# Kernel optimization log

Measured on AMD Instinct MI355X. Metric: run time of the kernel, lower is better.

Reference implementation:

```python
import jax, jax.numpy as jnp
import numpy as np

D = 256        # embedding dim (params[0])
V = 50000      # candidate vocab (params[1])
VW = 200000    # word vocab
B = 1024       # number of entities (batched ragged loop)
C = 64         # candidates per side (padded fixed length)
TOP_K = 10     # params[2]


def setup_inputs() -> dict:
    key = jax.random.key(0)
    ks = jax.random.split(key, 10)
    return {
        "word_l_ids": jax.random.randint(ks[0], (B,), 0, VW),
        "word_r_ids": jax.random.randint(ks[1], (B,), 0, VW),
        "cand_l_ids": jax.random.randint(ks[2], (B, C), 0, V),
        "cand_r_ids": jax.random.randint(ks[3], (B, C), 0, V),
        "word_embeds": jax.random.normal(ks[4], (VW, D), dtype=jnp.float32) * 0.1,
        "candidate_embeds": jax.random.normal(ks[5], (V, D), dtype=jnp.float32) * 0.1,
        # truncated_normal(stddev=0.5) for W_a, stddev=1.0 for W_c
        "W_a": jax.random.truncated_normal(ks[6], -2.0, 2.0, (D, D), dtype=jnp.float32) * 0.5,
        "b_a": jnp.zeros((1, D), dtype=jnp.float32),
        "W_c": jax.random.truncated_normal(ks[7], -2.0, 2.0, (2 * D, D), dtype=jnp.float32),
        "b_c": jnp.zeros((1, D), dtype=jnp.float32),
    }


def reference(word_l_ids, word_r_ids, cand_l_ids, cand_r_ids,
              word_embeds, candidate_embeds, W_a, b_a, W_c, b_c):
    # per-entity embedding lookups
    wl = word_embeds[word_l_ids]            # [B, D]
    wr = word_embeds[word_r_ids]            # [B, D]
    cl = candidate_embeds[cand_l_ids]       # [B, C, D]
    cr = candidate_embeds[cand_r_ids]       # [B, C, D]

    def attend(word, cands):
        # embed_word_align = tanh(word @ W_a + b_a)
        align = jnp.tanh(word @ W_a + b_a)                       # [B, D]
        # softmax over candidate axis (axis=0 in original per-entity view)
        scores = jnp.einsum("bcd,bd->bc", cands, align)          # [B, C]
        att = jax.nn.softmax(scores, axis=-1)                    # [B, C]
        # weighted sum of candidate embeddings
        return jnp.einsum("bc,bcd->bd", att, cands)              # [B, D]

    # note: left aggregation attends over RIGHT candidates and vice versa
    aggre_l = attend(wl, cr)
    aggre_r = attend(wr, cl)

    words_whole = wl + wr
    cands_whole = aggre_r + aggre_l
    phrase = jnp.tanh(jnp.concatenate([words_whole, cands_whole], axis=-1) @ W_c + b_c)  # [B, D]

    logits = phrase @ candidate_embeds.T    # [B, V]
    y_pred = jax.nn.softmax(logits, axis=-1)
    _, top_candidates = jax.lax.top_k(y_pred, TOP_K)             # [B, TOP_K]
    return y_pred, top_candidates
```

## Files before the change

### kernel.cpp

```cpp
#include <hip/hip_runtime.h>
#include <math.h>

#define DD 256
#define BB 1024
#define CC 64
#define VV 50000
#define TOPK 10
#define BM 128
#define BN 128
#define BK 64
#define LDK 72
#define NCHUNK 391
#define NMBLK 8
#define NWG (NCHUNK * NMBLK)
#define MAXCAND 60

typedef __attribute__((ext_vector_type(8))) short bf16x8;
typedef __attribute__((ext_vector_type(4))) float f32x4;

__device__ inline unsigned short f2bf(float x) {
    unsigned u = __float_as_uint(x);
    unsigned r = (u + 0x7FFFu + ((u >> 16) & 1u)) >> 16;
    return (unsigned short)r;
}

__global__ __launch_bounds__(256) void k_prep(
    const float* __restrict__ CE, unsigned short* __restrict__ CEb)
{
    const int i = blockIdx.x * 256 + threadIdx.x;
    const size_t base = (size_t)i * 8;
    if (base >= (size_t)VV * DD) return;
    const float4 a = *(const float4*)(CE + base);
    const float4 b = *(const float4*)(CE + base + 4);
    uint4 o;
    o.x = (unsigned)f2bf(a.x) | ((unsigned)f2bf(a.y) << 16);
    o.y = (unsigned)f2bf(a.z) | ((unsigned)f2bf(a.w) << 16);
    o.z = (unsigned)f2bf(b.x) | ((unsigned)f2bf(b.y) << 16);
    o.w = (unsigned)f2bf(b.z) | ((unsigned)f2bf(b.w) << 16);
    *(uint4*)(CEb + base) = o;
}

__global__ __launch_bounds__(256) void k_phrase(
    const int* __restrict__ wl_ids, const int* __restrict__ wr_ids,
    const int* __restrict__ cl_ids, const int* __restrict__ cr_ids,
    const float* __restrict__ WE, const float* __restrict__ CE,
    const float* __restrict__ W_a, const float* __restrict__ b_a,
    const float* __restrict__ W_c, const float* __restrict__ b_c,
    float* __restrict__ phrase, unsigned short* __restrict__ phraseb)
{
    const int b = blockIdx.x;
    const int t = threadIdx.x;
    __shared__ float s_wl[DD], s_wr[DD], s_align[DD], s_agg0[DD], s_agg1[DD];
    __shared__ float s_part[256];
    __shared__ float s_att[CC];
    __shared__ int s_rid[CC];

    s_wl[t] = WE[(size_t)wl_ids[b] * DD + t];
    s_wr[t] = WE[(size_t)wr_ids[b] * DD + t];
    __syncthreads();

    for (int side = 0; side < 2; ++side) {
        const float* w    = (side == 0) ? s_wl : s_wr;
        const int*   cids = (side == 0) ? (cr_ids + b * CC) : (cl_ids + b * CC);

        float acc = b_a[t];
        #pragma unroll 4
        for (int k = 0; k < DD; ++k) acc = fmaf(w[k], W_a[k * DD + t], acc);
        s_align[t] = tanhf(acc);
        if (t < CC) s_rid[t] = cids[t];
        __syncthreads();

        {
            const int c = t & 63, p = t >> 6;
            const float* crow = CE + (size_t)s_rid[c] * DD + p * 64;
            const float* al = s_align + p * 64;
            float sc = 0.f;
            #pragma unroll 4
            for (int j = 0; j < 64; ++j) sc = fmaf(crow[j], al[j], sc);
            s_part[t] = sc;
        }
        __syncthreads();
        if (t < CC) {
            float s = s_part[t] + s_part[64 + t] + s_part[128 + t] + s_part[192 + t];
            float m = s;
            for (int off = 32; off; off >>= 1) m = fmaxf(m, __shfl_xor(m, off, 64));
            float e = expf(s - m);
            float sum = e;
            for (int off = 32; off; off >>= 1) sum += __shfl_xor(sum, off, 64);
            s_att[t] = e / sum;
        }
        __syncthreads();
        {
            float ag = 0.f;
            #pragma unroll 4
            for (int c = 0; c < CC; ++c)
                ag = fmaf(s_att[c], CE[(size_t)s_rid[c] * DD + t], ag);
            if (side == 0) s_agg0[t] = ag; else s_agg1[t] = ag;
        }
        __syncthreads();
    }

    s_wl[t]  += s_wr[t];
    s_agg0[t] += s_agg1[t];
    __syncthreads();

    float acc = b_c[t];
    #pragma unroll 4
    for (int k = 0; k < DD; ++k) acc = fmaf(s_wl[k],  W_c[k * DD + t], acc);
    #pragma unroll 4
    for (int k = 0; k < DD; ++k) acc = fmaf(s_agg0[k], W_c[(DD + k) * DD + t], acc);
    const float ph = tanhf(acc);
    phrase[b * DD + t] = ph;
    phraseb[b * DD + t] = f2bf(ph);
}

template<bool STATS, bool BF16CE>
__global__ __launch_bounds__(256) void k_gemm(
    const unsigned short* __restrict__ phraseb,
    const float* __restrict__ CE, const unsigned short* __restrict__ CEb,
    float* __restrict__ out,
    float* __restrict__ pmax, float* __restrict__ psum,
    const float* __restrict__ rowM, const float* __restrict__ rowInvS,
    const float* __restrict__ rowTh,
    int* __restrict__ cand_idx, int* __restrict__ cand_cnt)
{
    __shared__ unsigned short sA[BM * LDK];
    __shared__ unsigned short sB[BN * LDK];

    const int t = threadIdx.x;
    const int wave = t >> 6, lane = t & 63;
    const int wm = wave >> 1, wn = wave & 1;
    const int quad = lane >> 4, l15 = lane & 15;

    const int wg = blockIdx.x;
    const int q  = (wg & 7) * NCHUNK + (wg >> 3);
    const int m0 = (q & 7) * BM;
    const int cn = q >> 3;
    const int n0 = cn * BN;

    f32x4 acc[4][4] = {};

    for (int k0 = 0; k0 < DD; k0 += BK) {
        __syncthreads();
        #pragma unroll
        for (int r = 0; r < 4; ++r) {
            const int idx = t + r * 256;
            const int m = idx >> 3, k8 = (idx & 7) * 8;
            const uint4 v = *(const uint4*)(phraseb + (size_t)(m0 + m) * DD + k0 + k8);
            *(uint4*)(sA + m * LDK + k8) = v;
        }
        if constexpr (BF16CE) {
            #pragma unroll
            for (int r = 0; r < 4; ++r) {
                const int idx = t + r * 256;
                const int n = idx >> 3, k8 = (idx & 7) * 8;
                const int gn = n0 + n;
                uint4 v = make_uint4(0u, 0u, 0u, 0u);
                if (gn < VV) v = *(const uint4*)(CEb + (size_t)gn * DD + k0 + k8);
                *(uint4*)(sB + n * LDK + k8) = v;
            }
        } else {
            #pragma unroll
            for (int r = 0; r < 8; ++r) {
                const int idx = t + r * 256;
                const int n = idx >> 4, k4 = (idx & 15) * 4;
                const int gn = n0 + n;
                float4 v = make_float4(0.f, 0.f, 0.f, 0.f);
                if (gn < VV) v = *(const float4*)(CE + (size_t)gn * DD + k0 + k4);
                ushort4 h;
                h.x = f2bf(v.x); h.y = f2bf(v.y); h.z = f2bf(v.z); h.w = f2bf(v.w);
                *(ushort4*)(sB + n * LDK + k4) = h;
            }
        }
        __syncthreads();
        #pragma unroll
        for (int kk = 0; kk < BK; kk += 32) {
            bf16x8 af[4], bfr[4];
            #pragma unroll
            for (int i = 0; i < 4; ++i) {
                af[i]  = *(const bf16x8*)(sA + (wm * 64 + i * 16 + l15) * LDK + kk + quad * 8);
                bfr[i] = *(const bf16x8*)(sB + (wn * 64 + i * 16 + l15) * LDK + kk + quad * 8);
            }
            #pragma unroll
            for (int i = 0; i < 4; ++i)
                #pragma unroll
                for (int j = 0; j < 4; ++j)
                    acc[i][j] = __builtin_amdgcn_mfma_f32_16x16x32_bf16(af[i], bfr[j], acc[i][j], 0, 0, 0);
        }
    }

    bool val[4];
    #pragma unroll
    for (int j = 0; j < 4; ++j) val[j] = (n0 + wn * 64 + j * 16 + l15) < VV;

    if constexpr (STATS) {
        __shared__ float sM[2][BM], sS[2][BM];
        #pragma unroll
        for (int i = 0; i < 4; ++i) {
            #pragma unroll
            for (int r = 0; r < 4; ++r) {
                float m1 = -INFINITY;
                #pragma unroll
                for (int j = 0; j < 4; ++j) if (val[j]) m1 = fmaxf(m1, acc[i][j][r]);
                #pragma unroll
                for (int off = 8; off >= 1; off >>= 1) m1 = fmaxf(m1, __shfl_xor(m1, off, 64));
                float s = 0.f;
                #pragma unroll
                for (int j = 0; j < 4; ++j) if (val[j]) s += __expf(acc[i][j][r] - m1);
                #pragma unroll
                for (int off = 8; off >= 1; off >>= 1) s += __shfl_xor(s, off, 64);
                if (l15 == 0) {
                    const int mloc = wm * 64 + i * 16 + quad * 4 + r;
                    sM[wn][mloc] = m1;
                    sS[wn][mloc] = s;
                }
            }
        }
        __syncthreads();
        if (t < BM) {
            const float Ma = sM[0][t], Mb = sM[1][t];
            const float nM = fmaxf(Ma, Mb);
            const float S  = sS[0][t] * __expf(Ma - nM) + sS[1][t] * __expf(Mb - nM);
            const size_t o = (size_t)(m0 + t) * NCHUNK + cn;
            pmax[o] = nM;
            psum[o] = S;
        }
    } else {
        __shared__ float sMr[BM], sIr[BM], sTr[BM];
        if (t < BM) {
            sMr[t] = rowM[m0 + t];
            sIr[t] = rowInvS[m0 + t];
            sTr[t] = rowTh[m0 + t];
        }
        __syncthreads();
        #pragma unroll
        for (int i = 0; i < 4; ++i) {
            #pragma unroll
            for (int r = 0; r < 4; ++r) {
                const int ml = wm * 64 + i * 16 + quad * 4 + r;
                const int gm = m0 + ml;
                const float M = sMr[ml], inv = sIr[ml], th = sTr[ml];
                #pragma unroll
                for (int j = 0; j < 4; ++j) {
                    if (val[j]) {
                        const int gn = n0 + wn * 64 + j * 16 + l15;
                        const float y = __expf(acc[i][j][r] - M) * inv;
                        __builtin_nontemporal_store(y, out + (size_t)gm * VV + gn);
                        if (y >= th) {
                            const int p = atomicAdd(&cand_cnt[gm], 1);
                            if (p < MAXCAND) cand_idx[gm * MAXCAND + p] = gn;
                        }
                    }
                }
            }
        }
    }
}

__global__ __launch_bounds__(64) void k_rowstats(
    const float* __restrict__ pmax, const float* __restrict__ psum,
    float* __restrict__ rowM, float* __restrict__ rowInvS, float* __restrict__ rowTh,
    int* __restrict__ cand_cnt)
{
    const int b = blockIdx.x, t = threadIdx.x;
    float M = -INFINITY, S = 0.f;
    float top[TOPK];
    #pragma unroll
    for (int j = 0; j < TOPK; ++j) top[j] = -INFINITY;

    for (int c = t; c < NCHUNK; c += 64) {
        const float m = pmax[(size_t)b * NCHUNK + c];
        const float s = psum[(size_t)b * NCHUNK + c];
        const float nM = fmaxf(M, m);
        S = S * __expf(M - nM) + s * __expf(m - nM);
        M = nM;
        if (m > top[TOPK - 1]) {
            float v = m;
            #pragma unroll
            for (int p = 0; p < TOPK; ++p) {
                const float hi = fmaxf(top[p], v), lo = fminf(top[p], v);
                top[p] = hi; v = lo;
            }
        }
    }
    #pragma unroll
    for (int off = 32; off; off >>= 1) {
        const float m2 = __shfl_xor(M, off, 64);
        const float s2 = __shfl_xor(S, off, 64);
        const float nM = fmaxf(M, m2);
        S = S * __expf(M - nM) + s2 * __expf(m2 - nM);
        M = nM;
    }
    float v10 = -INFINITY;
    for (int k = 0; k < TOPK; ++k) {
        float g = top[0];
        #pragma unroll
        for (int off = 32; off; off >>= 1) g = fmaxf(g, __shfl_xor(g, off, 64));
        v10 = g;
        const unsigned long long mk = __ballot(top[0] == g);
        if (mk && t == __ffsll(mk) - 1) {
            #pragma unroll
            for (int p = 0; p < TOPK - 1; ++p) top[p] = top[p + 1];
            top[TOPK - 1] = -INFINITY;
        }
    }
    if (t == 0) {
        rowM[b] = M;
        const float inv = 1.f / S;
        rowInvS[b] = inv;
        rowTh[b] = 0.90f * __expf(v10 - M) * inv;
        cand_cnt[b] = 0;
    }
}

__global__ __launch_bounds__(64) void k_rescore(
    const float* __restrict__ phrase, const float* __restrict__ CE,
    const int* __restrict__ cand_idx, const int* __restrict__ cand_cnt,
    float* __restrict__ topk_out)
{
    const int b = blockIdx.x, lane = threadIdx.x;
    int cnt = cand_cnt[b];
    if (cnt > MAXCAND) cnt = MAXCAND;
    __shared__ float s_val[MAXCAND];
    __shared__ int   s_idx[MAXCAND];

    if (lane < MAXCAND) { s_val[lane] = -INFINITY; s_idx[lane] = 0x7ffffff0; }
    __syncthreads();

    const float4 ph = *(const float4*)(phrase + (size_t)b * DD + lane * 4);
    for (int c = 0; c < cnt; ++c) {
        const int id = cand_idx[b * MAXCAND + c];
        const float4 ce = *(const float4*)(CE + (size_t)id * DD + lane * 4);
        float d = ph.x * ce.x + ph.y * ce.y + ph.z * ce.z + ph.w * ce.w;
        #pragma unroll
        for (int off = 32; off; off >>= 1) d += __shfl_xor(d, off, 64);
        if (lane == 0) { s_val[c] = d; s_idx[c] = id; }
    }
    __syncthreads();
    if (lane == 0) {
        for (int j = 0; j < TOPK; ++j) {
            int best = j;
            for (int c = j + 1; c < cnt; ++c) {
                if (s_val[c] > s_val[best] ||
                    (s_val[c] == s_val[best] && s_idx[c] < s_idx[best])) best = c;
            }
            const float bv = s_val[best]; const int bi = s_idx[best];
            s_val[best] = s_val[j]; s_idx[best] = s_idx[j];
            s_val[j] = bv; s_idx[j] = bi;
            topk_out[b * TOPK + j] = (float)bi;
        }
    }
}

extern "C" void kernel_launch(void* const* d_in, const int* in_sizes, int n_in,
                              void* d_out, int out_size, void* d_ws, size_t ws_size,
                              hipStream_t stream) {
    const int*   wl_ids = (const int*)d_in[0];
    const int*   wr_ids = (const int*)d_in[1];
    const int*   cl_ids = (const int*)d_in[2];
    const int*   cr_ids = (const int*)d_in[3];
    const float* WE     = (const float*)d_in[4];
    const float* CE     = (const float*)d_in[5];
    const float* W_a    = (const float*)d_in[6];
    const float* b_a    = (const float*)d_in[7];
    const float* W_c    = (const float*)d_in[8];
    const float* b_c    = (const float*)d_in[9];

    float* out = (float*)d_out;
    float* ws  = (float*)d_ws;

    float* phrase  = ws;
    unsigned short* phraseb = (unsigned short*)(ws + 262144);
    float* pmax    = ws + 262144 + 131072;
    float* psum    = pmax + (size_t)BB * NCHUNK;
    float* rowM    = psum + (size_t)BB * NCHUNK;
    float* rowInvS = rowM + BB;
    float* rowTh   = rowInvS + BB;
    int*   cand_idx = (int*)(rowTh + BB);
    int*   cand_cnt = cand_idx + (size_t)BB * MAXCAND;
    float* topk_out = out + (size_t)BB * VV;

    const size_t baseBytes = (size_t)((char*)(cand_cnt + BB) - (char*)ws);
    const size_t ceOff = (baseBytes + 255) & ~(size_t)255;
    const bool bf16ce = ws_size >= ceOff + (size_t)VV * DD * 2;
    unsigned short* CEb = (unsigned short*)((char*)ws + ceOff);

    k_phrase<<<BB, 256, 0, stream>>>(wl_ids, wr_ids, cl_ids, cr_ids,
                                     WE, CE, W_a, b_a, W_c, b_c, phrase, phraseb);
    if (bf16ce) {
        k_prep<<<(VV * DD / 8 + 255) / 256, 256, 0, stream>>>(CE, CEb);
        k_gemm<true, true><<<NWG, 256, 0, stream>>>(phraseb, CE, CEb, out,
            pmax, psum, rowM, rowInvS, rowTh, cand_idx, cand_cnt);
        k_rowstats<<<BB, 64, 0, stream>>>(pmax, psum, rowM, rowInvS, rowTh, cand_cnt);
        k_gemm<false, true><<<NWG, 256, 0, stream>>>(phraseb, CE, CEb, out,
            pmax, psum, rowM, rowInvS, rowTh, cand_idx, cand_cnt);
    } else {
        k_gemm<true, false><<<NWG, 256, 0, stream>>>(phraseb, CE, CEb, out,
            pmax, psum, rowM, rowInvS, rowTh, cand_idx, cand_cnt);
        k_rowstats<<<BB, 64, 0, stream>>>(pmax, psum, rowM, rowInvS, rowTh, cand_cnt);
        k_gemm<false, false><<<NWG, 256, 0, stream>>>(phraseb, CE, CEb, out,
            pmax, psum, rowM, rowInvS, rowTh, cand_idx, cand_cnt);
    }
    k_rescore<<<BB, 64, 0, stream>>>(phrase, CE, cand_idx, cand_cnt, topk_out);
}
```

Measured before the change: 696.0 us.

## Split phrase kernel into batched align, attention, and phrase GEMM kernels

```diff
diff --git a/kernel.cpp b/kernel.cpp
--- a/kernel.cpp
+++ b/kernel.cpp
@@ -112,6 +112,178 @@
     const float ph = tanhf(acc);
     phrase[b * DD + t] = ph;
     phraseb[b * DD + t] = f2bf(ph);
+}
+
+__global__ __launch_bounds__(256) void k_align(
+    const int* __restrict__ wl_ids, const int* __restrict__ wr_ids,
+    const float* __restrict__ WE,
+    const float* __restrict__ W_a, const float* __restrict__ b_a,
+    float* __restrict__ alignbuf, float* __restrict__ wordsum)
+{
+    __shared__ float sA[32][260];
+    __shared__ int s_id[32];
+
+    const int t  = threadIdx.x;
+    const int rt = blockIdx.x >> 2;
+    const int cg = blockIdx.x & 3;
+    const int b0 = rt * 16;
+    const int s0 = rt * 32;
+
+    if (t < 32) {
+        const int e = b0 + (t >> 1);
+        s_id[t] = (t & 1) ? wr_ids[e] : wl_ids[e];
+    }
+    __syncthreads();
+
+    #pragma unroll 8
+    for (int r = 0; r < 32; ++r)
+        sA[r][t] = WE[(size_t)s_id[r] * DD + t];
+    __syncthreads();
+
+    if (cg == 0) {
+        #pragma unroll
+        for (int i = 0; i < 16; ++i)
+            wordsum[(size_t)(b0 + i) * DD + t] = sA[2 * i][t] + sA[2 * i + 1][t];
+    }
+
+    const int c = t & 63, mg = t >> 6;
+    const int col = cg * 64 + c;
+    const float ba = b_a[col];
+    float acc[8];
+    #pragma unroll
+    for (int j = 0; j < 8; ++j) acc[j] = ba;
+
+    for (int k4 = 0; k4 < 64; ++k4) {
+        const int kb = k4 * 4;
+        const float w0 = W_a[(size_t)(kb + 0) * DD + col];
+        const float w1 = W_a[(size_t)(kb + 1) * DD + col];
+        const float w2 = W_a[(size_t)(kb + 2) * DD + col];
+        const float w3 = W_a[(size_t)(kb + 3) * DD + col];
+        #pragma unroll
+        for (int j = 0; j < 8; ++j) {
+            const float4 a = *(const float4*)&sA[mg * 8 + j][kb];
+            acc[j] = fmaf(a.x, w0, acc[j]);
+            acc[j] = fmaf(a.y, w1, acc[j]);
+            acc[j] = fmaf(a.z, w2, acc[j]);
+            acc[j] = fmaf(a.w, w3, acc[j]);
+        }
+    }
+    #pragma unroll
+    for (int j = 0; j < 8; ++j)
+        alignbuf[(size_t)(s0 + mg * 8 + j) * DD + col] = tanhf(acc[j]);
+}
+
+__global__ __launch_bounds__(256) void k_attn(
+    const int* __restrict__ cl_ids, const int* __restrict__ cr_ids,
+    const float* __restrict__ CE, const float* __restrict__ alignbuf,
+    float* __restrict__ aggsum)
+{
+    __shared__ float sC[CC][260];
+    __shared__ float sAl[DD];
+    __shared__ float s_part[256];
+    __shared__ float s_att[CC];
+    __shared__ int s_rid[CC];
+
+    const int b = blockIdx.x;
+    const int t = threadIdx.x;
+    float agg_acc = 0.f;
+
+    for (int side = 0; side < 2; ++side) {
+        const int* cids = (side == 0) ? (cr_ids + b * CC) : (cl_ids + b * CC);
+        if (t < CC) s_rid[t] = cids[t];
+        sAl[t] = alignbuf[(size_t)(2 * b + side) * DD + t];
+        __syncthreads();
+
+        #pragma unroll 8
+        for (int r = 0; r < CC; ++r)
+            sC[r][t] = CE[(size_t)s_rid[r] * DD + t];
+        __syncthreads();
+
+        {
+            const int c = t & 63, p = t >> 6;
+            float sc = 0.f;
+            #pragma unroll
+            for (int jj = 0; jj < 16; ++jj) {
+                const float4 v  = *(const float4*)&sC[c][p * 64 + 4 * jj];
+                const float4 al = *(const float4*)&sAl[p * 64 + 4 * jj];
+                sc = fmaf(v.x, al.x, sc);
+                sc = fmaf(v.y, al.y, sc);
+                sc = fmaf(v.z, al.z, sc);
+                sc = fmaf(v.w, al.w, sc);
+            }
+            s_part[t] = sc;
+        }
+        __syncthreads();
+        if (t < CC) {
+            float s = s_part[t] + s_part[64 + t] + s_part[128 + t] + s_part[192 + t];
+            float m = s;
+            for (int off = 32; off; off >>= 1) m = fmaxf(m, __shfl_xor(m, off, 64));
+            float e = expf(s - m);
+            float sum = e;
+            for (int off = 32; off; off >>= 1) sum += __shfl_xor(sum, off, 64);
+            s_att[t] = e / sum;
+        }
+        __syncthreads();
+        {
+            float ag = 0.f;
+            #pragma unroll 8
+            for (int c = 0; c < CC; ++c)
+                ag = fmaf(s_att[c], sC[c][t], ag);
+            agg_acc += ag;
+        }
+        __syncthreads();
+    }
+    aggsum[(size_t)b * DD + t] = agg_acc;
+}
+
+__global__ __launch_bounds__(256) void k_phrase2(
+    const float* __restrict__ wordsum, const float* __restrict__ aggsum,
+    const float* __restrict__ W_c, const float* __restrict__ b_c,
+    float* __restrict__ phrase, unsigned short* __restrict__ phraseb)
+{
+    __shared__ float sX[16][516];
+
+    const int t  = threadIdx.x;
+    const int rt = blockIdx.x >> 2;
+    const int cg = blockIdx.x & 3;
+    const int b0 = rt * 16;
+
+    #pragma unroll
+    for (int i = 0; i < 16; ++i) {
+        sX[i][t]       = wordsum[(size_t)(b0 + i) * DD + t];
+        sX[i][DD + t]  = aggsum [(size_t)(b0 + i) * DD + t];
+    }
+    __syncthreads();
+
+    const int c = t & 63, mg = t >> 6;
+    const int col = cg * 64 + c;
+    const float bc = b_c[col];
+    float acc[4];
+    #pragma unroll
+    for (int j = 0; j < 4; ++j) acc[j] = bc;
+
+    for (int k4 = 0; k4 < 128; ++k4) {
+        const int kb = k4 * 4;
+        const float w0 = W_c[(size_t)(kb + 0) * DD + col];
+        const float w1 = W_c[(size_t)(kb + 1) * DD + col];
+        const float w2 = W_c[(size_t)(kb + 2) * DD + col];
+        const float w3 = W_c[(size_t)(kb + 3) * DD + col];
+        #pragma unroll
+        for (int j = 0; j < 4; ++j) {
+            const float4 a = *(const float4*)&sX[mg * 4 + j][kb];
+            acc[j] = fmaf(a.x, w0, acc[j]);
+            acc[j] = fmaf(a.y, w1, acc[j]);
+            acc[j] = fmaf(a.z, w2, acc[j]);
+            acc[j] = fmaf(a.w, w3, acc[j]);
+        }
+    }
+    #pragma unroll
+    for (int j = 0; j < 4; ++j) {
+        const int b = b0 + mg * 4 + j;
+        const float ph = tanhf(acc[j]);
+        phrase[(size_t)b * DD + col] = ph;
+        phraseb[(size_t)b * DD + col] = f2bf(ph);
+    }
 }
 
 template<bool STATS, bool BF16CE>
@@ -381,12 +553,25 @@
     float* topk_out = out + (size_t)BB * VV;
 
     const size_t baseBytes = (size_t)((char*)(cand_cnt + BB) - (char*)ws);
-    const size_t ceOff = (baseBytes + 255) & ~(size_t)255;
+
+    float* alignbuf = (float*)((char*)ws + baseBytes);
+    float* wordsum  = alignbuf + (size_t)2 * BB * DD;
+    float* aggsum   = wordsum + (size_t)BB * DD;
+    const size_t ext1End = baseBytes + (size_t)4 * BB * DD * 4;
+    const bool newphrase = ws_size >= ext1End;
+
+    const size_t ceOff = ((newphrase ? ext1End : baseBytes) + 255) & ~(size_t)255;
     const bool bf16ce = ws_size >= ceOff + (size_t)VV * DD * 2;
     unsigned short* CEb = (unsigned short*)((char*)ws + ceOff);
 
-    k_phrase<<<BB, 256, 0, stream>>>(wl_ids, wr_ids, cl_ids, cr_ids,
-                                     WE, CE, W_a, b_a, W_c, b_c, phrase, phraseb);
+    if (newphrase) {
+        k_align<<<256, 256, 0, stream>>>(wl_ids, wr_ids, WE, W_a, b_a, alignbuf, wordsum);
+        k_attn<<<BB, 256, 0, stream>>>(cl_ids, cr_ids, CE, alignbuf, aggsum);
+        k_phrase2<<<256, 256, 0, stream>>>(wordsum, aggsum, W_c, b_c, phrase, phraseb);
+    } else {
+        k_phrase<<<BB, 256, 0, stream>>>(wl_ids, wr_ids, cl_ids, cr_ids,
+                                         WE, CE, W_a, b_a, W_c, b_c, phrase, phraseb);
+    }
     if (bf16ce) {
         k_prep<<<(VV * DD / 8 + 255) / 256, 256, 0, stream>>>(CE, CEb);
         k_gemm<true, true><<<NWG, 256, 0, stream>>>(phraseb, CE, CEb, out,
```

New measurement: 654.8 us. 1.06x faster.
